# Kernel tuning notes

Measured on AMD Instinct MI355X. Metric: run time of the kernel, lower is better.

The kernel has to match this reference:

```python
import jax, jax.numpy as jnp
import numpy as np

N = 8192
IN_F = 256
HEADS = 4
HF = 64            # head_features = out_features / heads
OUT_F = HEADS * HF # concat=True
NEG_SLOPE = 0.2


def setup_inputs() -> dict:
    key = jax.random.key(0)
    ks = jax.random.split(key, 7)
    x = jax.random.normal(ks[0], (N, IN_F), dtype=jnp.float32)
    graph = jax.random.randint(ks[1], (N, N), 0, 2, dtype=jnp.int32)
    weight = jax.random.normal(ks[2], (HEADS, IN_F, HF), dtype=jnp.float32) * (1.0 / np.sqrt(IN_F))
    weight_i = jax.random.normal(ks[3], (HEADS, HF, 1), dtype=jnp.float32) * (1.0 / np.sqrt(HF))
    weight_j = jax.random.normal(ks[4], (HEADS, HF, 1), dtype=jnp.float32) * (1.0 / np.sqrt(HF))
    weight_r = jax.random.normal(ks[5], (IN_F, HF * HEADS), dtype=jnp.float32) * (1.0 / np.sqrt(IN_F))
    bias = jnp.zeros((OUT_F,), dtype=jnp.float32)
    return {"x": x, "graph": graph, "weight": weight, "weight_i": weight_i,
            "weight_j": weight_j, "weight_r": weight_r, "bias": bias}


def reference(x, graph, weight, weight_i, weight_j, weight_r, bias):
    # h: per-head projected features [heads, N, hf]
    h = jnp.einsum('nm,hmf->hnf', x, weight)
    # additive attention logits: coe_i [h,N,1] + coe_j [h,1,N]
    coe_i = jnp.einsum('hnf,hfo->hno', h, weight_i)          # [heads, N, 1]
    coe_j = jnp.einsum('hnf,hfo->hno', h, weight_j)          # [heads, N, 1]
    coe = jax.nn.leaky_relu(coe_i + jnp.swapaxes(coe_j, 1, 2), NEG_SLOPE)  # [heads, N, N]
    # adjacency mask (note transpose, matching the torch code)
    mask = jnp.where(graph > 0, 0.0, -jnp.inf).T             # [N, N]
    att = jax.nn.softmax(coe + mask[None], axis=-1)          # [heads, N, N]
    # aggregate and move heads to axis 1: [N, heads, hf]
    y = jnp.einsum('hij,hjf->ihf', att, h)
    # residual with projection (in_features != head_features)
    y = y + (x @ weight_r).reshape(N, HEADS, HF)
    # concat heads + bias
    y = y.reshape(N, OUT_F) + bias
    return y
```

## Files before the change

### kernel.cpp

```cpp
#include <hip/hip_runtime.h>
#include <hip/hip_bf16.h>

#define N 8192
#define IN_F 256
#define HEADS 4
#define HF 64
#define OUT_F 256

typedef __attribute__((ext_vector_type(8))) short short8;
typedef __attribute__((ext_vector_type(4))) float f32x4;

__device__ __forceinline__ float lrelu(float x) {
    return fmaxf(x, 0.0f) * 0.8f + x * 0.2f;
}
__device__ __forceinline__ short f2bf(float f) {
    union { __hip_bfloat16 h; short s; } u;
    u.h = __float2bfloat16(f);
    return u.s;
}
__device__ __forceinline__ float bf2f(unsigned short b) {
    union { unsigned u; float f; } v; v.u = ((unsigned)b) << 16;
    return v.f;
}
__device__ __forceinline__ unsigned pack_bf16(float p0, float p1) {
    union { __hip_bfloat162 b; unsigned u; } cv;
    cv.b = __float22bfloat162_rn(make_float2(p0, p1));
    return cv.u;
}

#define GLOAD_LDS(gsrc, ldst) \
    __builtin_amdgcn_global_load_lds( \
        (const __attribute__((address_space(1))) void*)(gsrc), \
        (__attribute__((address_space(3))) void*)(ldst), 16, 0, 0)

__global__ __launch_bounds__(256) void k_wcvt(
    const float* __restrict__ w, const float* __restrict__ wr,
    unsigned short* __restrict__ BbT)
{
    int c = blockIdx.x;
    int k = threadIdx.x;
    float v;
    if (c < 256) {
        int head = c >> 6, f = c & 63;
        v = w[((size_t)head * IN_F + k) * HF + f];
    } else {
        v = wr[(size_t)k * OUT_F + (c - 256)];
    }
    BbT[(size_t)c * IN_F + k] = (unsigned short)f2bf(v);
}

__global__ __launch_bounds__(256) void k_gemm_pack(
    const float* __restrict__ x, const unsigned short* __restrict__ BbT,
    const float* __restrict__ bias,
    unsigned short* __restrict__ hT, float* __restrict__ out,
    const int* __restrict__ graph, unsigned int* __restrict__ bits)
{
    __shared__ unsigned short Asw[64 * 64];
    __shared__ unsigned short Bsw[128 * 64];
    int b = blockIdx.x;
    int t = threadIdx.x;

    if (b >= 512) {
        int p = b - 512;
        int jw = p & 255;
        int i = (p >> 8) * 256 + t;
        const int* gp = graph + (size_t)(jw * 32) * N + i;
        unsigned int word = 0;
        #pragma unroll
        for (int k = 0; k < 32; ++k)
            word |= (gp[(size_t)k * N] > 0 ? 1u : 0u) << k;
        bits[(size_t)jw * N + i] = word;
        return;
    }

    int m0 = (b & 127) * 64;
    int bn = b >> 7;
    int w_ = t >> 6, l = t & 63;
    int wr_ = w_ >> 1, wc_ = w_ & 1;
    int ar = l & 15, g = l >> 4;

    f32x4 acc[2][4];
    #pragma unroll
    for (int m = 0; m < 2; ++m)
        #pragma unroll
        for (int n = 0; n < 4; ++n) acc[m][n] = (f32x4){0.f, 0.f, 0.f, 0.f};

    int srow = t >> 2, skq = (t & 3) * 16;
    int sc = t >> 1, sh = (t & 1) * 32;

    for (int kt = 0; kt < 4; ++kt) {
        const float* xs = x + (size_t)(m0 + srow) * IN_F + kt * 64 + skq;
        float4 xa = ((const float4*)xs)[0];
        float4 xb = ((const float4*)xs)[1];
        float4 xc = ((const float4*)xs)[2];
        float4 xd = ((const float4*)xs)[3];
        unsigned ae[8];
        ae[0] = pack_bf16(xa.x, xa.y); ae[1] = pack_bf16(xa.z, xa.w);
        ae[2] = pack_bf16(xb.x, xb.y); ae[3] = pack_bf16(xb.z, xb.w);
        ae[4] = pack_bf16(xc.x, xc.y); ae[5] = pack_bf16(xc.z, xc.w);
        ae[6] = pack_bf16(xd.x, xd.y); ae[7] = pack_bf16(xd.z, xd.w);
        int kb0 = (skq >> 3) ^ (srow & 7);
        int kb1 = ((skq >> 3) + 1) ^ (srow & 7);
        *(uint4*)&Asw[srow * 64 + kb0 * 8] = *(uint4*)&ae[0];
        *(uint4*)&Asw[srow * 64 + kb1 * 8] = *(uint4*)&ae[4];
        const unsigned short* bs = BbT + (size_t)(bn * 128 + sc) * IN_F + kt * 64 + sh;
        uint4 b0 = ((const uint4*)bs)[0];
        uint4 b1 = ((const uint4*)bs)[1];
        uint4 b2 = ((const uint4*)bs)[2];
        uint4 b3 = ((const uint4*)bs)[3];
        int hb = sh >> 3;
        *(uint4*)&Bsw[sc * 64 + ((hb + 0) ^ (sc & 7)) * 8] = b0;
        *(uint4*)&Bsw[sc * 64 + ((hb + 1) ^ (sc & 7)) * 8] = b1;
        *(uint4*)&Bsw[sc * 64 + ((hb + 2) ^ (sc & 7)) * 8] = b2;
        *(uint4*)&Bsw[sc * 64 + ((hb + 3) ^ (sc & 7)) * 8] = b3;
        __syncthreads();
        #pragma unroll
        for (int ks = 0; ks < 2; ++ks) {
            short8 af[2], bf[4];
            #pragma unroll
            for (int m = 0; m < 2; ++m) {
                int row = wr_ * 32 + m * 16 + ar;
                int kb = (ks * 4 + g) ^ (row & 7);
                af[m] = *(const short8*)&Asw[row * 64 + kb * 8];
            }
            #pragma unroll
            for (int n = 0; n < 4; ++n) {
                int c = wc_ * 64 + n * 16 + ar;
                int kb = (ks * 4 + g) ^ (c & 7);
                bf[n] = *(const short8*)&Bsw[c * 64 + kb * 8];
            }
            #pragma unroll
            for (int m = 0; m < 2; ++m)
                #pragma unroll
                for (int n = 0; n < 4; ++n)
                    acc[m][n] = __builtin_amdgcn_mfma_f32_16x16x32_bf16(af[m], bf[n], acc[m][n], 0, 0, 0);
        }
        __syncthreads();
    }
    #pragma unroll
    for (int m = 0; m < 2; ++m) {
        #pragma unroll
        for (int n = 0; n < 4; ++n) {
            int cg = bn * 128 + wc_ * 64 + n * 16 + ar;
            int mg0 = m0 + wr_ * 32 + m * 16 + g * 4;
            if (cg < 256) {
                int head = cg >> 6, f = cg & 63;
                unsigned pk[2];
                pk[0] = pack_bf16(acc[m][n][0], acc[m][n][1]);
                pk[1] = pack_bf16(acc[m][n][2], acc[m][n][3]);
                *(uint2*)(hT + (size_t)(head * HF + f) * N + mg0) = *(uint2*)pk;
            } else {
                float bb = bias[cg - 256];
                #pragma unroll
                for (int r = 0; r < 4; ++r)
                    out[(size_t)(mg0 + r) * OUT_F + (cg - 256)] = acc[m][n][r] + bb;
            }
        }
    }
}

__global__ __launch_bounds__(256) void k_coe(
    const unsigned short* __restrict__ hT, const float* __restrict__ wi,
    const float* __restrict__ wj, float* __restrict__ coe_i, float* __restrict__ coe_j)
{
    int head = blockIdx.y;
    int n = blockIdx.x * 256 + threadIdx.x;
    const unsigned short* hp = hT + (size_t)head * HF * N + n;
    float si = 0.f, sj = 0.f;
    #pragma unroll 8
    for (int f = 0; f < HF; ++f) {
        float hv = bf2f(hp[(size_t)f * N]);
        si = fmaf(hv, wi[head * HF + f], si);
        sj = fmaf(hv, wj[head * HF + f], sj);
    }
    coe_i[head * N + n] = si;
    coe_j[head * N + n] = sj;
}

__global__ __launch_bounds__(256) void k_cols(
    const float* __restrict__ coe_j, float* __restrict__ maxB,
    float* __restrict__ F, float* __restrict__ H)
{
    __shared__ float red[256];
    int head = blockIdx.x;
    int t = threadIdx.x;
    float m = -1e30f;
    for (int n = t; n < N; n += 256) {
        float b = coe_j[head * N + n];
        F[head * N + n] = __expf(b);
        H[head * N + n] = __expf(0.2f * b);
        m = fmaxf(m, b);
    }
    red[t] = m;
    __syncthreads();
    for (int s = 128; s > 0; s >>= 1) {
        if (t < s) red[t] = fmaxf(red[t], red[t + s]);
        __syncthreads();
    }
    if (t == 0) maxB[head] = red[0];
}

__device__ __forceinline__ short8 makeP(
    const float4& fa, const float4& fb4, const float4& ha, const float4& hb4,
    unsigned int mk, float Ei, float Gi)
{
    float fv[8] = {fa.x, fa.y, fa.z, fa.w, fb4.x, fb4.y, fb4.z, fb4.w};
    float hv[8] = {ha.x, ha.y, ha.z, ha.w, hb4.x, hb4.y, hb4.z, hb4.w};
    union { short8 s8; unsigned u[4]; } A;
    #pragma unroll
    for (int jp = 0; jp < 4; ++jp) {
        float p0 = fmaxf(Ei * fv[2 * jp],     Gi * hv[2 * jp]);
        float p1 = fmaxf(Ei * fv[2 * jp + 1], Gi * hv[2 * jp + 1]);
        int s0 = __builtin_amdgcn_sbfe((int)mk, 2 * jp, 1);
        int s1 = __builtin_amdgcn_sbfe((int)mk, 2 * jp + 1, 1);
        p0 = __int_as_float(__float_as_int(p0) & s0);
        p1 = __int_as_float(__float_as_int(p1) & s1);
        A.u[jp] = pack_bf16(p0, p1);
    }
    return A.s8;
}

__global__ __launch_bounds__(512) void k_att(
    const unsigned short* __restrict__ hT, const float* __restrict__ coe_i,
    const float* __restrict__ maxB, const float* __restrict__ F,
    const float* __restrict__ H, const unsigned int* __restrict__ bits,
    float* __restrict__ out)
{
    __shared__ char smem[65536];
    unsigned short* hb = (unsigned short*)smem;
    float* mbuf = (float*)smem;

    int t = threadIdx.x;
    int head = blockIdx.y;
    int i0 = blockIdx.x * 64;
    int w = t >> 6, l = t & 63;
    int rg = w >> 2, grp = w & 3;
    int ar = l & 15, g = l >> 4, g8 = g * 8;

    int irow0 = i0 + rg * 32 + ar;
    int irow1 = irow0 + 16;
    float mB = maxB[head];
    float a0 = coe_i[head * N + irow0];
    float a1 = coe_i[head * N + irow1];
    float M0 = lrelu(a0 + mB);
    float M1 = lrelu(a1 + mB);
    float Ei0 = __expf(a0 - M0), Gi0 = __expf(0.2f * a0 - M0);
    float Ei1 = __expf(a1 - M1), Gi1 = __expf(0.2f * a1 - M1);

    f32x4 acc0[4], acc1[4];
    #pragma unroll
    for (int fb = 0; fb < 4; ++fb) {
        acc0[fb] = (f32x4){0.f, 0.f, 0.f, 0.f};
        acc1[fb] = (f32x4){0.f, 0.f, 0.f, 0.f};
    }
    f32x4 accd0 = (f32x4){0.f, 0.f, 0.f, 0.f};
    f32x4 accd1 = (f32x4){0.f, 0.f, 0.f, 0.f};

    short8 ones;
    #pragma unroll
    for (int k = 0; k < 8; ++k) ones[k] = (short)0x3F80;

    int tg = w >> 1;
    int rb0 = (w & 1) * 32;
    int lrow = l >> 3;
    int slot = l & 7;
    int gg = slot ^ lrow;
    const unsigned short* qsrc[4];
    #pragma unroll
    for (int q = 0; q < 4; ++q) {
        int sf = rb0 + q * 8 + lrow;
        qsrc[q] = hT + (size_t)(head * HF + sf) * N + tg * 64 + gg * 8;
    }
    int ldsoff0 = tg * 4096 + rb0 * 64;

    const float* Fp = F + head * N + g8;
    const float* Hp = H + head * N + g8;
    const unsigned int* bp0 = bits + irow0;
    const unsigned int* bp1 = bits + irow1;

    #pragma unroll
    for (int q = 0; q < 4; ++q)
        GLOAD_LDS(qsrc[q], hb + ldsoff0 + q * 512);

    for (int s = 0; s < 32; ++s) {
        int jt = s * 256 + grp * 64;
        size_t jwd = (size_t)(jt >> 5);
        unsigned int mk00 = bp0[jwd * N] >> g8;
        unsigned int mk01 = bp0[(jwd + 1) * N] >> g8;
        unsigned int mk10 = bp1[jwd * N] >> g8;
        unsigned int mk11 = bp1[(jwd + 1) * N] >> g8;
        float4 fa0 = *(const float4*)(Fp + jt);
        float4 fb0 = *(const float4*)(Fp + jt + 4);
        float4 ha0 = *(const float4*)(Hp + jt);
        float4 hb0 = *(const float4*)(Hp + jt + 4);
        float4 fa1 = *(const float4*)(Fp + jt + 32);
        float4 fb1 = *(const float4*)(Fp + jt + 36);
        float4 ha1 = *(const float4*)(Hp + jt + 32);
        float4 hb1 = *(const float4*)(Hp + jt + 36);
        short8 af00 = makeP(fa0, fb0, ha0, hb0, mk00, Ei0, Gi0);
        short8 af10 = makeP(fa0, fb0, ha0, hb0, mk10, Ei1, Gi1);
        short8 af01 = makeP(fa1, fb1, ha1, hb1, mk01, Ei0, Gi0);
        short8 af11 = makeP(fa1, fb1, ha1, hb1, mk11, Ei1, Gi1);

        __syncthreads();

        if (s < 31) {
            int bon = ((s + 1) & 1) * 16384;
            int jn = (s + 1) * 256;
            #pragma unroll
            for (int q = 0; q < 4; ++q)
                GLOAD_LDS(qsrc[q] + jn, hb + bon + ldsoff0 + q * 512);
        }

        int bo = (s & 1) * 16384;
        const unsigned short* rbuf = &hb[bo + grp * 4096];
        #pragma unroll
        for (int ss = 0; ss < 2; ++ss) {
            short8 a0f = ss ? af01 : af00;
            short8 a1f = ss ? af11 : af10;
            #pragma unroll
            for (int fb = 0; fb < 4; ++fb) {
                int row = fb * 16 + ar;
                int pg = (ss * 4 + g) ^ (ar & 7);
                short8 bfr = *(const short8*)&rbuf[row * 64 + pg * 8];
                acc0[fb] = __builtin_amdgcn_mfma_f32_16x16x32_bf16(a0f, bfr, acc0[fb], 0, 0, 0);
                acc1[fb] = __builtin_amdgcn_mfma_f32_16x16x32_bf16(a1f, bfr, acc1[fb], 0, 0, 0);
            }
            accd0 = __builtin_amdgcn_mfma_f32_16x16x32_bf16(a0f, ones, accd0, 0, 0, 0);
            accd1 = __builtin_amdgcn_mfma_f32_16x16x32_bf16(a1f, ones, accd1, 0, 0, 0);
        }
    }

    __syncthreads();
    int slot_m = rg * 64 + l;
    if (grp > 0) {
        float* dst = mbuf + (size_t)(grp - 1) * 5248 + slot_m * 41;
        #pragma unroll
        for (int fb = 0; fb < 4; ++fb)
            #pragma unroll
            for (int r = 0; r < 4; ++r) {
                dst[fb * 4 + r] = acc0[fb][r];
                dst[16 + fb * 4 + r] = acc1[fb][r];
            }
        #pragma unroll
        for (int r = 0; r < 4; ++r) {
            dst[32 + r] = accd0[r];
            dst[36 + r] = accd1[r];
        }
    }
    __syncthreads();
    if (grp == 0) {
        #pragma unroll
        for (int q = 0; q < 3; ++q) {
            const float* src = mbuf + (size_t)q * 5248 + slot_m * 41;
            #pragma unroll
            for (int fb = 0; fb < 4; ++fb)
                #pragma unroll
                for (int r = 0; r < 4; ++r) {
                    acc0[fb][r] += src[fb * 4 + r];
                    acc1[fb][r] += src[16 + fb * 4 + r];
                }
            #pragma unroll
            for (int r = 0; r < 4; ++r) {
                accd0[r] += src[32 + r];
                accd1[r] += src[36 + r];
            }
        }
        #pragma unroll
        for (int r = 0; r < 4; ++r) {
            float inv0 = 1.0f / accd0[r];
            float inv1 = 1.0f / accd1[r];
            int orow0 = i0 + rg * 32 + g * 4 + r;
            float* op0 = out + (size_t)orow0 * OUT_F + head * HF + ar;
            float* op1 = op0 + 16 * OUT_F;
            #pragma unroll
            for (int fb = 0; fb < 4; ++fb) {
                op0[fb * 16] += acc0[fb][r] * inv0;
                op1[fb * 16] += acc1[fb][r] * inv1;
            }
        }
    }
}

extern "C" void kernel_launch(void* const* d_in, const int* in_sizes, int n_in,
                              void* d_out, int out_size, void* d_ws, size_t ws_size,
                              hipStream_t stream) {
    const float* x     = (const float*)d_in[0];
    const int*   graph = (const int*)d_in[1];
    const float* w     = (const float*)d_in[2];
    const float* wi    = (const float*)d_in[3];
    const float* wj    = (const float*)d_in[4];
    const float* wr    = (const float*)d_in[5];
    const float* bias  = (const float*)d_in[6];
    float* out = (float*)d_out;

    char* ws = (char*)d_ws;
    unsigned short* hT  = (unsigned short*)(ws);
    float* coe_i = (float*)(ws + 4194304);
    float* coe_j = (float*)(ws + 4325376);
    float* maxB  = (float*)(ws + 4456448);
    float* F     = (float*)(ws + 4457472);
    float* H     = (float*)(ws + 4588544);
    unsigned short* BbT = (unsigned short*)(ws + 4719616);
    unsigned int* bits  = (unsigned int*)(ws + 4981760);

    k_wcvt<<<dim3(512), 256, 0, stream>>>(w, wr, BbT);
    k_gemm_pack<<<dim3(512 + 8192), 256, 0, stream>>>(x, BbT, bias, hT, out, graph, bits);
    k_coe<<<dim3(32, 4), 256, 0, stream>>>(hT, wi, wj, coe_i, coe_j);
    k_cols<<<dim3(4), 256, 0, stream>>>(coe_j, maxB, F, H);
    k_att<<<dim3(N / 64, HEADS), 512, 0, stream>>>(hT, coe_i, maxB, F, H, bits, out);
}
```

Measured before the change: 164.0 us.

## Fuse attention-coefficient dot products into GEMM epilogue and prefetch mask bits

```diff
diff --git a/kernel.cpp b/kernel.cpp
--- a/kernel.cpp
+++ b/kernel.cpp
@@ -51,8 +51,10 @@
 
 __global__ __launch_bounds__(256) void k_gemm_pack(
     const float* __restrict__ x, const unsigned short* __restrict__ BbT,
-    const float* __restrict__ bias,
+    const float* __restrict__ bias, const float* __restrict__ wi,
+    const float* __restrict__ wj,
     unsigned short* __restrict__ hT, float* __restrict__ out,
+    float* __restrict__ coe_i, float* __restrict__ coe_j,
     const int* __restrict__ graph, unsigned int* __restrict__ bits)
 {
     __shared__ unsigned short Asw[64 * 64];
@@ -157,24 +159,45 @@
             }
         }
     }
-}
-
-__global__ __launch_bounds__(256) void k_coe(
-    const unsigned short* __restrict__ hT, const float* __restrict__ wi,
-    const float* __restrict__ wj, float* __restrict__ coe_i, float* __restrict__ coe_j)
-{
-    int head = blockIdx.y;
-    int n = blockIdx.x * 256 + threadIdx.x;
-    const unsigned short* hp = hT + (size_t)head * HF * N + n;
-    float si = 0.f, sj = 0.f;
-    #pragma unroll 8
-    for (int f = 0; f < HF; ++f) {
-        float hv = bf2f(hp[(size_t)f * N]);
-        si = fmaf(hv, wi[head * HF + f], si);
-        sj = fmaf(hv, wj[head * HF + f], sj);
-    }
-    coe_i[head * N + n] = si;
-    coe_j[head * N + n] = sj;
+    if (bn < 2) {
+        int head = bn * 2 + wc_;
+        float pi[2][4], pj[2][4];
+        #pragma unroll
+        for (int m = 0; m < 2; ++m)
+            #pragma unroll
+            for (int r = 0; r < 4; ++r) { pi[m][r] = 0.f; pj[m][r] = 0.f; }
+        #pragma unroll
+        for (int n = 0; n < 4; ++n) {
+            float wiv = wi[head * HF + n * 16 + ar];
+            float wjv = wj[head * HF + n * 16 + ar];
+            #pragma unroll
+            for (int m = 0; m < 2; ++m)
+                #pragma unroll
+                for (int r = 0; r < 4; ++r) {
+                    pi[m][r] = fmaf(acc[m][n][r], wiv, pi[m][r]);
+                    pj[m][r] = fmaf(acc[m][n][r], wjv, pj[m][r]);
+                }
+        }
+        #pragma unroll
+        for (int o = 1; o <= 8; o <<= 1)
+            #pragma unroll
+            for (int m = 0; m < 2; ++m)
+                #pragma unroll
+                for (int r = 0; r < 4; ++r) {
+                    pi[m][r] += __shfl_xor(pi[m][r], o, 64);
+                    pj[m][r] += __shfl_xor(pj[m][r], o, 64);
+                }
+        if (ar == 0) {
+            #pragma unroll
+            for (int m = 0; m < 2; ++m)
+                #pragma unroll
+                for (int r = 0; r < 4; ++r) {
+                    int row = m0 + wr_ * 32 + m * 16 + g * 4 + r;
+                    coe_i[head * N + row] = pi[m][r];
+                    coe_j[head * N + row] = pj[m][r];
+                }
+        }
+    }
 }
 
 __global__ __launch_bounds__(256) void k_cols(
@@ -281,14 +304,18 @@
     #pragma unroll
     for (int q = 0; q < 4; ++q)
         GLOAD_LDS(qsrc[q], hb + ldsoff0 + q * 512);
+    unsigned mk00, mk01, mk10, mk11;
+    {
+        int jt0 = grp * 64;
+        size_t jw0 = (size_t)(jt0 >> 5);
+        mk00 = bp0[jw0 * N] >> g8;
+        mk01 = bp0[(jw0 + 1) * N] >> g8;
+        mk10 = bp1[jw0 * N] >> g8;
+        mk11 = bp1[(jw0 + 1) * N] >> g8;
+    }
 
     for (int s = 0; s < 32; ++s) {
         int jt = s * 256 + grp * 64;
-        size_t jwd = (size_t)(jt >> 5);
-        unsigned int mk00 = bp0[jwd * N] >> g8;
-        unsigned int mk01 = bp0[(jwd + 1) * N] >> g8;
-        unsigned int mk10 = bp1[jwd * N] >> g8;
-        unsigned int mk11 = bp1[(jwd + 1) * N] >> g8;
         float4 fa0 = *(const float4*)(Fp + jt);
         float4 fb0 = *(const float4*)(Fp + jt + 4);
         float4 ha0 = *(const float4*)(Hp + jt);
@@ -311,6 +338,12 @@
             for (int q = 0; q < 4; ++q)
                 GLOAD_LDS(qsrc[q] + jn, hb + bon + ldsoff0 + q * 512);
         }
+        int sn = (s + 1 < 32) ? s + 1 : s;
+        size_t jwn = (size_t)(((size_t)sn * 256 + grp * 64) >> 5);
+        unsigned nk00 = bp0[jwn * N] >> g8;
+        unsigned nk01 = bp0[(jwn + 1) * N] >> g8;
+        unsigned nk10 = bp1[jwn * N] >> g8;
+        unsigned nk11 = bp1[(jwn + 1) * N] >> g8;
 
         int bo = (s & 1) * 16384;
         const unsigned short* rbuf = &hb[bo + grp * 4096];
@@ -329,6 +362,7 @@
             accd0 = __builtin_amdgcn_mfma_f32_16x16x32_bf16(a0f, ones, accd0, 0, 0, 0);
             accd1 = __builtin_amdgcn_mfma_f32_16x16x32_bf16(a1f, ones, accd1, 0, 0, 0);
         }
+        mk00 = nk00; mk01 = nk01; mk10 = nk10; mk11 = nk11;
     }
 
     __syncthreads();
@@ -405,8 +439,7 @@
     unsigned int* bits  = (unsigned int*)(ws + 4981760);
 
     k_wcvt<<<dim3(512), 256, 0, stream>>>(w, wr, BbT);
-    k_gemm_pack<<<dim3(512 + 8192), 256, 0, stream>>>(x, BbT, bias, hT, out, graph, bits);
-    k_coe<<<dim3(32, 4), 256, 0, stream>>>(hT, wi, wj, coe_i, coe_j);
+    k_gemm_pack<<<dim3(512 + 8192), 256, 0, stream>>>(x, BbT, bias, wi, wj, hT, out, coe_i, coe_j, graph, bits);
     k_cols<<<dim3(4), 256, 0, stream>>>(coe_j, maxB, F, H);
     k_att<<<dim3(N / 64, HEADS), 512, 0, stream>>>(hT, coe_i, maxB, F, H, bits, out);
 }
```

Measured after the change: 157.9 us. 1.04x faster.
